# Performance work log

Hardware: AMD Instinct MI355X
Metric: run time of the kernel (lower is better)

## Reference

```python
import jax, jax.numpy as jnp
import numpy as np


def spmm(src, dst, w, x, n):
    # out[i] = sum_{e: dst[e]==i} w[e] * x[src[e]]  == th.spmm(adj, x) with adj COO (dst=row, src=col)
    return jax.ops.segment_sum(x[src] * w[:, None], dst, num_segments=n)


def gcn(x, ei, w, W1, b1, W2, b2):
    # GCN.forward: relu(gc1(x, adj)) -> dropout(eval: identity) -> gc2(x, adj)
    n = x.shape[0]
    src, dst = ei[1], ei[0]
    h = jax.nn.relu(spmm(src, dst, w, x @ W1, n) + b1)
    return spmm(src, dst, w, h @ W2, n) + b2


def setup_inputs() -> dict:
    key = jax.random.key(0)
    ks = jax.random.split(key, 24)
    Nd, Ns = 100000, 50000
    Fd, Fs, H1, H2 = 256, 256, 256, 128
    DEG = 32
    Ed, Es = Nd * DEG, Ns * DEG
    inp = {}
    inp['drug_sim_feat'] = jax.random.normal(ks[0], (Nd, Fd), jnp.float32)
    inp['drug_edge_index'] = jax.random.randint(ks[1], (2, Ed), 0, Nd, jnp.int32)
    inp['drug_edge_weight'] = jax.random.uniform(ks[2], (Ed,), jnp.float32) / DEG
    inp['drug_feat_edge_index'] = jax.random.randint(ks[3], (2, Ed), 0, Nd, jnp.int32)
    inp['drug_feat_edge_weight'] = jax.random.uniform(ks[4], (Ed,), jnp.float32) / DEG
    inp['disease_sim_feat'] = jax.random.normal(ks[5], (Ns, Fs), jnp.float32)
    inp['dis_edge_index'] = jax.random.randint(ks[6], (2, Es), 0, Ns, jnp.int32)
    inp['dis_edge_weight'] = jax.random.uniform(ks[7], (Es,), jnp.float32) / DEG
    inp['dis_feat_edge_index'] = jax.random.randint(ks[8], (2, Es), 0, Ns, jnp.int32)
    inp['dis_feat_edge_weight'] = jax.random.uniform(ks[9], (Es,), jnp.float32) / DEG
    # params: uniform(-stdv, stdv), stdv = 1/sqrt(out_features) as in reset_parameters
    def unif(k, shape, out_f):
        s = 1.0 / np.sqrt(out_f)
        return jax.random.uniform(k, shape, jnp.float32, -s, s)
    inp['W1d'] = unif(ks[10], (Fd, H1), H1); inp['b1d'] = unif(ks[11], (H1,), H1)
    inp['W2d'] = unif(ks[12], (H1, H2), H2); inp['b2d'] = unif(ks[13], (H2,), H2)
    inp['W1s'] = unif(ks[14], (Fs, H1), H1); inp['b1s'] = unif(ks[15], (H1,), H1)
    inp['W2s'] = unif(ks[16], (H1, H2), H2); inp['b2s'] = unif(ks[17], (H2,), H2)
    # fusion Linears (nhid2*2 -> nhid2); kaiming-ish uniform
    fs = 1.0 / np.sqrt(2 * H2)
    inp['Wfd'] = jax.random.uniform(ks[18], (2 * H2, H2), jnp.float32, -fs, fs)
    inp['bfd'] = jax.random.uniform(ks[19], (H2,), jnp.float32, -fs, fs)
    inp['Wfs'] = jax.random.uniform(ks[20], (2 * H2, H2), jnp.float32, -fs, fs)
    inp['bfs'] = jax.random.uniform(ks[21], (H2,), jnp.float32, -fs, fs)
    return inp


def reference(drug_sim_feat, drug_edge_index, drug_edge_weight,
              drug_feat_edge_index, drug_feat_edge_weight,
              disease_sim_feat, dis_edge_index, dis_edge_weight,
              dis_feat_edge_index, dis_feat_edge_weight,
              W1d, b1d, W2d, b2d, W1s, b1s, W2s, b2s,
              Wfd, bfd, Wfs, bfs):
    # dropout in eval mode (identity)
    emb1_sim = gcn(drug_sim_feat, drug_edge_index, drug_edge_weight, W1d, b1d, W2d, b2d)
    emb2_sim = gcn(disease_sim_feat, dis_edge_index, dis_edge_weight, W1s, b1s, W2s, b2s)
    emb1_feat = gcn(drug_sim_feat, drug_feat_edge_index, drug_feat_edge_weight, W1d, b1d, W2d, b2d)
    emb2_feat = gcn(disease_sim_feat, dis_feat_edge_index, dis_feat_edge_weight, W1s, b1s, W2s, b2s)
    emb1 = jax.nn.relu(jnp.concatenate([emb1_sim, emb1_feat], axis=1) @ Wfd + bfd)
    emb2 = jax.nn.relu(jnp.concatenate([emb2_sim, emb2_feat], axis=1) @ Wfs + bfs)
    return (emb1, emb2, emb1_sim, emb1_feat, emb2_sim, emb2_feat)
```

## Files before the change

### kernel.cpp

```cpp
#include <hip/hip_runtime.h>

typedef _Float16 f16;
typedef __attribute__((ext_vector_type(8))) _Float16 f16x8;
typedef __attribute__((ext_vector_type(4))) float f32x4;

__device__ inline ushort f2h_bits(float f) {
    f16 h = (f16)f;
    return __builtin_bit_cast(ushort, h);
}

struct T6 {
    const float* s[6];
    ushort* d[6];
    int N[6];
};

__global__ __launch_bounds__(256) void transpose6_k(T6 a) {
    __shared__ ushort tile[32][33];
    const int z = blockIdx.z;
    const int K = 256, N = a.N[z];
    int k0 = blockIdx.x * 32, n0 = blockIdx.y * 32;
    if (n0 >= N) return;
    const float* W = a.s[z];
    ushort* Wt = a.d[z];
    int tx = threadIdx.x & 31, ty = threadIdx.x >> 5;
    #pragma unroll
    for (int i = 0; i < 32; i += 8)
        tile[ty + i][tx] = f2h_bits(W[(size_t)(k0 + ty + i) * N + n0 + tx]);
    __syncthreads();
    #pragma unroll
    for (int i = 0; i < 32; i += 8)
        Wt[(size_t)(n0 + ty + i) * K + k0 + tx] = tile[tx][ty + i];
}

struct GraphDesc {
    const int* ei;
    const float* w;
    int E, n, NB, bstoff;
    int* row_ptr;
    int2* perm;
};
struct G4 { GraphDesc g[4]; };

__global__ __launch_bounds__(256) void hist_b(G4 a, int* __restrict__ bcounts) {
    const GraphDesc& G = a.g[blockIdx.y];
    const int e0 = blockIdx.x * 4096;
    if (e0 >= G.E) return;
    __shared__ int h[512];
    int t = threadIdx.x;
    h[t] = 0; h[t + 256] = 0;
    __syncthreads();
    #pragma unroll
    for (int k = 0; k < 16; ++k) {
        int i = e0 + t + k * 256;
        if (i < G.E) atomicAdd(&h[((uint)G.ei[i]) >> 8], 1);
    }
    __syncthreads();
    int* bc = bcounts + blockIdx.y * 512;
    for (int b = t; b < 512; b += 256)
        if (h[b]) atomicAdd(&bc[b], h[b]);
}

__global__ __launch_bounds__(256) void scan_b(G4 a, const int* __restrict__ bcounts,
                                              int* __restrict__ bbase, int* __restrict__ bcursor) {
    const int gidx = blockIdx.x;
    const GraphDesc& G = a.g[gidx];
    const int* bc = bcounts + gidx * 512;
    int* base = bbase + gidx * 513;
    int* cur  = bcursor + gidx * 512;
    int t = threadIdx.x, lane = t & 63, wave = t >> 6;
    int v0 = bc[2 * t], v1 = bc[2 * t + 1];
    int s = v0 + v1;
    int incl = s;
    for (int off = 1; off < 64; off <<= 1) {
        int u = __shfl_up(incl, off);
        if (lane >= off) incl += u;
    }
    __shared__ int wsum[4];
    if (lane == 63) wsum[wave] = incl;
    __syncthreads();
    int excl = incl - s;
    for (int wv = 0; wv < wave; ++wv) excl += wsum[wv];
    base[2 * t] = excl;      cur[2 * t] = excl;
    base[2 * t + 1] = excl + v0; cur[2 * t + 1] = excl + v0;
    if (t == 0) { base[512] = G.E; G.row_ptr[G.n] = G.E; }
}

__global__ __launch_bounds__(256) void scatter_b(G4 a, int* __restrict__ bcursor,
                                                 int2* __restrict__ bst) {
    const GraphDesc& G = a.g[blockIdx.y];
    const int e0 = blockIdx.x * 4096;
    if (e0 >= G.E) return;
    __shared__ int hist[512], excl[512], sbase[512], lcur[512];
    __shared__ int2 stage[4096];
    __shared__ ushort sbin[4096];
    const int t = threadIdx.x, lane = t & 63, wave = t >> 6;
    const int cnt = min(4096, G.E - e0);
    int* bcur = bcursor + blockIdx.y * 512;

    hist[t] = 0; hist[t + 256] = 0;
    __syncthreads();

    int   d[16], s[16];
    float wv[16];
    #pragma unroll
    for (int k = 0; k < 16; ++k) {
        int i = t + k * 256;
        if (i < cnt) {
            d[k]  = G.ei[e0 + i];
            s[k]  = G.ei[(size_t)G.E + e0 + i];
            wv[k] = G.w[e0 + i];
            atomicAdd(&hist[((uint)d[k]) >> 8], 1);
        }
    }
    __syncthreads();

    {
        int v0 = hist[2 * t], v1 = hist[2 * t + 1];
        int sum = v0 + v1;
        int incl = sum;
        for (int off = 1; off < 64; off <<= 1) {
            int u = __shfl_up(incl, off);
            if (lane >= off) incl += u;
        }
        __shared__ int wsum[4];
        if (lane == 63) wsum[wave] = incl;
        __syncthreads();
        int e = incl - sum;
        for (int wvv = 0; wvv < wave; ++wvv) e += wsum[wvv];
        excl[2 * t] = e; excl[2 * t + 1] = e + v0;
    }
    __syncthreads();

    for (int b = t; b < 512; b += 256) {
        int c = hist[b];
        sbase[b] = c ? atomicAdd(&bcur[b], c) : 0;
        lcur[b] = excl[b];
    }
    __syncthreads();

    #pragma unroll
    for (int k = 0; k < 16; ++k) {
        int i = t + k * 256;
        if (i < cnt) {
            int bin = ((uint)d[k]) >> 8;
            int pos = atomicAdd(&lcur[bin], 1);
            stage[pos] = make_int2((s[k] << 8) | (d[k] & 255), __float_as_int(wv[k]));
            sbin[pos] = (ushort)bin;
        }
    }
    __syncthreads();

    #pragma unroll
    for (int k = 0; k < 16; ++k) {
        int i = t + k * 256;
        if (i < cnt) {
            int2 r = stage[i];
            int bin = sbin[i];
            bst[(size_t)G.bstoff + sbase[bin] + i - excl[bin]] = r;
        }
    }
}

__global__ __launch_bounds__(256) void finalize_b(G4 a, const int* __restrict__ bbase,
                                                  const int2* __restrict__ bst) {
    const GraphDesc& G = a.g[blockIdx.y];
    const int b = blockIdx.x;
    if (b >= G.NB) return;
    __shared__ int hist[256], cur[256], wsum[4];
    const int t = threadIdx.x, lane = t & 63, wave = t >> 6;
    const int* base = bbase + blockIdx.y * 513;
    const int lo = base[b], hi = base[b + 1];
    const int2* bg = bst + G.bstoff;
    hist[t] = 0;
    __syncthreads();
    for (int i = lo + t; i < hi; i += 256)
        atomicAdd(&hist[bg[i].x & 255], 1);
    __syncthreads();
    int v = hist[t];
    int incl = v;
    for (int off = 1; off < 64; off <<= 1) {
        int u = __shfl_up(incl, off);
        if (lane >= off) incl += u;
    }
    if (lane == 63) wsum[wave] = incl;
    __syncthreads();
    int excl = incl - v;
    for (int wv = 0; wv < wave; ++wv) excl += wsum[wv];
    const int r0 = b << 8;
    const int nrows = min(256, G.n - r0);
    if (t < nrows) G.row_ptr[r0 + t] = lo + excl;
    cur[t] = lo + excl;
    __syncthreads();
    for (int i = lo + t; i < hi; i += 256) {
        int2 r = bg[i];
        int local = r.x & 255;
        int slot = atomicAdd(&cur[local], 1);
        G.perm[slot] = make_int2(r.x >> 8, r.y);
    }
}

template<int C, bool RELU, bool DUAL>
__global__ __launch_bounds__(256) void spmm_f16(
    const f16* __restrict__ x,
    const int2* __restrict__ perm,
    const int* __restrict__ row_ptr, const float* __restrict__ bias,
    ushort* __restrict__ out_h, float* __restrict__ out_f, int n)
{
    const int wave = threadIdx.x >> 6, lane = threadIdx.x & 63;
    const int row = blockIdx.x * 4 + wave;
    if (row >= n) return;
    const int F = 64 * C;
    const int e0 = row_ptr[row], e1 = row_ptr[row + 1];
    float acc[C] = {};
    const int laneoff = lane * C;

    for (int eb = e0; eb < e1; eb += 64) {
        int idx = eb + lane;
        int myS = 0; int myW = 0;
        if (idx < e1) { int2 rec = perm[idx]; myS = rec.x; myW = rec.y; }
        int m = min(64, e1 - eb);
        for (int j0 = 0; j0 < m; j0 += 8) {
            #pragma unroll
            for (int u = 0; u < 8; ++u) {
                int j = j0 + u;
                int   s = __builtin_amdgcn_readlane(myS, j);
                float w = __int_as_float(__builtin_amdgcn_readlane(myW, j));
                const f16* xr = x + (size_t)((uint)s * (uint)F) + laneoff;
                if (C == 4) {
                    union { uint2 u2; f16 h[4]; } cv;
                    cv.u2 = *reinterpret_cast<const uint2*>(xr);
                    acc[0] = fmaf((float)cv.h[0], w, acc[0]);
                    acc[1] = fmaf((float)cv.h[1], w, acc[1]);
                    acc[2] = fmaf((float)cv.h[2], w, acc[2]);
                    acc[3] = fmaf((float)cv.h[3], w, acc[3]);
                } else {
                    union { uint u1; f16 h[2]; } cv;
                    cv.u1 = *reinterpret_cast<const uint*>(xr);
                    acc[0] = fmaf((float)cv.h[0], w, acc[0]);
                    acc[1] = fmaf((float)cv.h[1], w, acc[1]);
                }
            }
        }
    }

    #pragma unroll
    for (int c = 0; c < C; ++c) {
        float v = acc[c] + bias[laneoff + c];
        acc[c] = RELU ? fmaxf(v, 0.f) : v;
    }
    size_t ob = (size_t)row * F + laneoff;
    if (DUAL) {
        if (C == 4) *reinterpret_cast<float4*>(out_f + ob) = make_float4(acc[0], acc[1], acc[2], acc[3]);
        else        *reinterpret_cast<float2*>(out_f + ob) = make_float2(acc[0], acc[1]);
    }
    if (C == 4) *reinterpret_cast<ushort4*>(out_h + ob) =
        make_ushort4(f2h_bits(acc[0]), f2h_bits(acc[1]), f2h_bits(acc[2]), f2h_bits(acc[3]));
    else        *reinterpret_cast<ushort2*>(out_h + ob) =
        make_ushort2(f2h_bits(acc[0]), f2h_bits(acc[1]));
}

template<bool CVTA, bool FUSE, bool RELU, bool BIAS, bool F32OUT>
__global__ __launch_bounds__(256) void gemm_mfma(
    const void* __restrict__ Av, const ushort* __restrict__ A2,
    const ushort* __restrict__ Bt, const float* __restrict__ bias,
    ushort* __restrict__ Ch, float* __restrict__ Cf,
    int M, int N, int K)
{
    __shared__ ushort Asb[128 * 32];
    __shared__ ushort Bsb[128 * 32];
    const int tid = threadIdx.x;
    const int lane = tid & 63, wave = tid >> 6;
    const int wr = wave >> 1, wc = wave & 1;
    const int bm = blockIdx.x * 128, bn = blockIdx.y * 128;

    f32x4 acc[4][4] = {};

    for (int k0 = 0; k0 < K; k0 += 32) {
        #pragma unroll
        for (int h = 0; h < 2; ++h) {
            int slot = tid + 256 * h;
            int r = slot >> 2, cb = slot & 3;
            int row = bm + r;
            uint4 v = make_uint4(0, 0, 0, 0);
            if (row < M) {
                int kk = k0 + cb * 8;
                if (CVTA) {
                    const float* Af = (const float*)Av;
                    float4 lo = *reinterpret_cast<const float4*>(Af + (size_t)row * K + kk);
                    float4 hi = *reinterpret_cast<const float4*>(Af + (size_t)row * K + kk + 4);
                    ushort h8[8] = { f2h_bits(lo.x), f2h_bits(lo.y), f2h_bits(lo.z), f2h_bits(lo.w),
                                     f2h_bits(hi.x), f2h_bits(hi.y), f2h_bits(hi.z), f2h_bits(hi.w) };
                    v = *reinterpret_cast<const uint4*>(h8);
                } else if (FUSE) {
                    const ushort* Ap = (kk < 128) ? (const ushort*)Av : A2;
                    v = *reinterpret_cast<const uint4*>(Ap + (size_t)row * 128 + (kk & 127));
                } else {
                    v = *reinterpret_cast<const uint4*>((const ushort*)Av + (size_t)row * K + kk);
                }
            }
            int scb = cb ^ ((r >> 1) & 3);
            *reinterpret_cast<uint4*>(&Asb[r * 32 + scb * 8]) = v;
        }
        #pragma unroll
        for (int h = 0; h < 2; ++h) {
            int slot = tid + 256 * h;
            int r = slot >> 2, cb = slot & 3;
            uint4 v = *reinterpret_cast<const uint4*>(Bt + (size_t)(bn + r) * K + k0 + cb * 8);
            int scb = cb ^ ((r >> 1) & 3);
            *reinterpret_cast<uint4*>(&Bsb[r * 32 + scb * 8]) = v;
        }
        __syncthreads();

        f16x8 fa[4], fb[4];
        #pragma unroll
        for (int i = 0; i < 4; ++i) {
            int r = wr * 64 + i * 16 + (lane & 15);
            int scb = (lane >> 4) ^ ((r >> 1) & 3);
            fa[i] = *reinterpret_cast<const f16x8*>(&Asb[r * 32 + scb * 8]);
        }
        #pragma unroll
        for (int j = 0; j < 4; ++j) {
            int r = wc * 64 + j * 16 + (lane & 15);
            int scb = (lane >> 4) ^ ((r >> 1) & 3);
            fb[j] = *reinterpret_cast<const f16x8*>(&Bsb[r * 32 + scb * 8]);
        }
        #pragma unroll
        for (int i = 0; i < 4; ++i)
            #pragma unroll
            for (int j = 0; j < 4; ++j)
                acc[i][j] = __builtin_amdgcn_mfma_f32_16x16x32_f16(fa[i], fb[j], acc[i][j], 0, 0, 0);
        __syncthreads();
    }

    #pragma unroll
    for (int i = 0; i < 4; ++i) {
        #pragma unroll
        for (int r4 = 0; r4 < 4; ++r4) {
            int row = bm + wr * 64 + i * 16 + (lane >> 4) * 4 + r4;
            if (row >= M) continue;
            #pragma unroll
            for (int j = 0; j < 4; ++j) {
                int col = bn + wc * 64 + j * 16 + (lane & 15);
                float v = acc[i][j][r4];
                if (BIAS) v += bias[col];
                if (RELU) v = fmaxf(v, 0.f);
                if (F32OUT) Cf[(size_t)row * N + col] = v;
                else        Ch[(size_t)row * N + col] = f2h_bits(v);
            }
        }
    }
}

extern "C" void kernel_launch(void* const* d_in, const int* in_sizes, int n_in,
                              void* d_out, int out_size, void* d_ws, size_t ws_size,
                              hipStream_t stream) {
    const float* Xd       = (const float*)d_in[0];
    const int*   eid_sim  = (const int*)  d_in[1];
    const float* wd_sim   = (const float*)d_in[2];
    const int*   eid_feat = (const int*)  d_in[3];
    const float* wd_feat  = (const float*)d_in[4];
    const float* Xs       = (const float*)d_in[5];
    const int*   eis_sim  = (const int*)  d_in[6];
    const float* ws_sim   = (const float*)d_in[7];
    const int*   eis_feat = (const int*)  d_in[8];
    const float* ws_feat  = (const float*)d_in[9];
    const float* W1d = (const float*)d_in[10]; const float* b1d = (const float*)d_in[11];
    const float* W2d = (const float*)d_in[12]; const float* b2d = (const float*)d_in[13];
    const float* W1s = (const float*)d_in[14]; const float* b1s = (const float*)d_in[15];
    const float* W2s = (const float*)d_in[16]; const float* b2s = (const float*)d_in[17];
    const float* Wfd = (const float*)d_in[18]; const float* bfd = (const float*)d_in[19];
    const float* Wfs = (const float*)d_in[20]; const float* bfs = (const float*)d_in[21];

    const int Fd = 256, H1 = 256, H2 = 128;
    const int Nd = in_sizes[0] / Fd;
    const int Ns = in_sizes[5] / Fd;
    const int Ed = in_sizes[2];
    const int Es = in_sizes[7];

    float* out    = (float*)d_out;
    float* o_emb1 = out;
    float* o_emb2 = o_emb1 + (size_t)Nd * H2;
    float* o_e1s  = o_emb2 + (size_t)Ns * H2;
    float* o_e1f  = o_e1s  + (size_t)Nd * H2;
    float* o_e2s  = o_e1f  + (size_t)Nd * H2;
    float* o_e2f  = o_e2s  + (size_t)Ns * H2;

    char* p = (char*)d_ws;
    auto alloc = [&](size_t bytes) { char* q = p; p += (bytes + 255) & ~(size_t)255; return q; };
    ushort* xw1   = (ushort*)alloc((size_t)Nd * 256 * 2);
    ushort* hbuf  = (ushort*)alloc((size_t)Nd * 256 * 2);
    ushort* tbuf  = (ushort*)alloc((size_t)Nd * 128 * 2);
    ushort* es_h  = (ushort*)alloc((size_t)Nd * 128 * 2);
    ushort* ef_h  = (ushort*)alloc((size_t)Nd * 128 * 2);
    ushort* W1dt  = (ushort*)alloc(256 * 256 * 2);
    ushort* W2dt  = (ushort*)alloc(256 * 128 * 2);
    ushort* Wfdt  = (ushort*)alloc(256 * 128 * 2);
    ushort* W1st  = (ushort*)alloc(256 * 256 * 2);
    ushort* W2st  = (ushort*)alloc(256 * 128 * 2);
    ushort* Wfst  = (ushort*)alloc(256 * 128 * 2);
    int2*   perm0 = (int2*)alloc((size_t)Ed * 8);
    int2*   perm1 = (int2*)alloc((size_t)Ed * 8);
    int2*   perm2 = (int2*)alloc((size_t)Es * 8);
    int2*   perm3 = (int2*)alloc((size_t)Es * 8);
    int*    rp0   = (int*) alloc((size_t)(Nd + 1) * 4);
    int*    rp1   = (int*) alloc((size_t)(Nd + 1) * 4);
    int*    rp2   = (int*) alloc((size_t)(Ns + 1) * 4);
    int*    rp3   = (int*) alloc((size_t)(Ns + 1) * 4);
    int*    bcounts = (int*)alloc(4 * 512 * 4);
    int*    bbase   = (int*)alloc(4 * 513 * 4);
    int*    bcursor = (int*)alloc(4 * 512 * 4);
    int2*   bst     = (int2*)xw1;

    {
        T6 a;
        a.s[0] = W1d; a.s[1] = W2d; a.s[2] = Wfd; a.s[3] = W1s; a.s[4] = W2s; a.s[5] = Wfs;
        a.d[0] = W1dt; a.d[1] = W2dt; a.d[2] = Wfdt; a.d[3] = W1st; a.d[4] = W2st; a.d[5] = Wfst;
        a.N[0] = 256; a.N[1] = 128; a.N[2] = 128; a.N[3] = 256; a.N[4] = 128; a.N[5] = 128;
        transpose6_k<<<dim3(8, 8, 6), 256, 0, stream>>>(a);
    }

    G4 a;
    a.g[0] = { eid_sim,  wd_sim,  Ed, Nd, (Nd + 255) >> 8, 0,           rp0, perm0 };
    a.g[1] = { eid_feat, wd_feat, Ed, Nd, (Nd + 255) >> 8, Ed,          rp1, perm1 };
    a.g[2] = { eis_sim,  ws_sim,  Es, Ns, (Ns + 255) >> 8, 2 * Ed,      rp2, perm2 };
    a.g[3] = { eis_feat, ws_feat, Es, Ns, (Ns + 255) >> 8, 2 * Ed + Es, rp3, perm3 };
    {
        const int maxEB = (Ed + 4095) / 4096;
        const int maxNB = (Nd + 255) >> 8;
        hipMemsetAsync(bcounts, 0, 4 * 512 * 4, stream);
        hist_b<<<dim3(maxEB, 4), 256, 0, stream>>>(a, bcounts);
        scan_b<<<4, 256, 0, stream>>>(a, bcounts, bbase, bcursor);
        scatter_b<<<dim3(maxEB, 4), 256, 0, stream>>>(a, bcursor, bst);
        finalize_b<<<dim3(maxNB, 4), 256, 0, stream>>>(a, bbase, bst);
    }

    auto branch = [&](const float* X, int n,
                      const int2* pA, const int* rpA,
                      const int2* pB, const int* rpB,
                      const ushort* W1t, const float* b1,
                      const ushort* W2t, const float* b2,
                      const ushort* Wft, const float* bfu,
                      float* o_sim, float* o_feat, float* o_emb) {
        gemm_mfma<true, false, false, false, false><<<dim3((n + 127) / 128, 2), 256, 0, stream>>>(
            X, nullptr, W1t, nullptr, xw1, nullptr, n, 256, 256);
        const int2* pm[2] = {pA, pB};
        const int*  rp[2] = {rpA, rpB};
        float*      of[2] = {o_sim, o_feat};
        ushort*     oh[2] = {es_h, ef_h};
        for (int g = 0; g < 2; ++g) {
            spmm_f16<4, true, false><<<(n + 3) / 4, 256, 0, stream>>>(
                (const f16*)xw1, pm[g], rp[g], b1, hbuf, nullptr, n);
            gemm_mfma<false, false, false, false, false><<<dim3((n + 127) / 128, 1), 256, 0, stream>>>(
                hbuf, nullptr, W2t, nullptr, tbuf, nullptr, n, 128, 256);
            spmm_f16<2, false, true><<<(n + 3) / 4, 256, 0, stream>>>(
                (const f16*)tbuf, pm[g], rp[g], b2, oh[g], of[g], n);
        }
        gemm_mfma<false, true, true, true, true><<<dim3((n + 127) / 128, 1), 256, 0, stream>>>(
            es_h, ef_h, Wft, bfu, nullptr, o_emb, n, 128, 256);
    };

    branch(Xd, Nd, perm0, rp0, perm1, rp1,
           W1dt, b1d, W2dt, b2d, Wfdt, bfd, o_e1s, o_e1f, o_emb1);
    branch(Xs, Ns, perm2, rp2, perm3, rp3,
           W1st, b1s, W2st, b2s, Wfst, bfs, o_e2s, o_e2f, o_emb2);
}
```

Measured before the change: 1.384 ms.

## Batch both graphs' layer-1 SpMM into one launch and swap GEMM grid order

The two layer-1 SpMMs, which share the same XW1 input, now run as a single launch with blockIdx.y selecting the graph, writing into separate h buffers so both graphs gather from XW1 in the same window. The first GEMM's grid is swapped so the two N-tiles of one M block run adjacently and can share the A rows. The SpMM kernel is split into specialised layer-1 and layer-2 versions. Workspace is reshuffled to make room for the second h/t buffers, which adds memory footprint and aliases es_h/ef_h onto xw1.

```diff
diff --git a/kernel.cpp b/kernel.cpp
--- a/kernel.cpp
+++ b/kernel.cpp
@@ -200,18 +200,24 @@
     }
 }
 
-template<int C, bool RELU, bool DUAL>
-__global__ __launch_bounds__(256) void spmm_f16(
-    const f16* __restrict__ x,
-    const int2* __restrict__ perm,
-    const int* __restrict__ row_ptr, const float* __restrict__ bias,
-    ushort* __restrict__ out_h, float* __restrict__ out_f, int n)
+struct PairDesc {
+    const int2* perm[2];
+    const int*  rp[2];
+    ushort*     outh[2];
+};
+
+template<int C>
+__global__ __launch_bounds__(256) void spmm_pair_f16(
+    const f16* __restrict__ x, PairDesc a, const float* __restrict__ bias, int n)
 {
+    const int g = blockIdx.y;
     const int wave = threadIdx.x >> 6, lane = threadIdx.x & 63;
     const int row = blockIdx.x * 4 + wave;
     if (row >= n) return;
+    const int2* __restrict__ perm = a.perm[g];
+    const int*  __restrict__ rp   = a.rp[g];
     const int F = 64 * C;
-    const int e0 = row_ptr[row], e1 = row_ptr[row + 1];
+    const int e0 = rp[row], e1 = rp[row + 1];
     float acc[C] = {};
     const int laneoff = lane * C;
 
@@ -227,19 +233,12 @@
                 int   s = __builtin_amdgcn_readlane(myS, j);
                 float w = __int_as_float(__builtin_amdgcn_readlane(myW, j));
                 const f16* xr = x + (size_t)((uint)s * (uint)F) + laneoff;
-                if (C == 4) {
-                    union { uint2 u2; f16 h[4]; } cv;
-                    cv.u2 = *reinterpret_cast<const uint2*>(xr);
-                    acc[0] = fmaf((float)cv.h[0], w, acc[0]);
-                    acc[1] = fmaf((float)cv.h[1], w, acc[1]);
-                    acc[2] = fmaf((float)cv.h[2], w, acc[2]);
-                    acc[3] = fmaf((float)cv.h[3], w, acc[3]);
-                } else {
-                    union { uint u1; f16 h[2]; } cv;
-                    cv.u1 = *reinterpret_cast<const uint*>(xr);
-                    acc[0] = fmaf((float)cv.h[0], w, acc[0]);
-                    acc[1] = fmaf((float)cv.h[1], w, acc[1]);
-                }
+                union { uint2 u2; f16 h[4]; } cv;
+                cv.u2 = *reinterpret_cast<const uint2*>(xr);
+                acc[0] = fmaf((float)cv.h[0], w, acc[0]);
+                acc[1] = fmaf((float)cv.h[1], w, acc[1]);
+                acc[2] = fmaf((float)cv.h[2], w, acc[2]);
+                acc[3] = fmaf((float)cv.h[3], w, acc[3]);
             }
         }
     }
@@ -247,20 +246,53 @@
     #pragma unroll
     for (int c = 0; c < C; ++c) {
         float v = acc[c] + bias[laneoff + c];
-        acc[c] = RELU ? fmaxf(v, 0.f) : v;
-    }
+        acc[c] = fmaxf(v, 0.f);
+    }
+    *reinterpret_cast<ushort4*>(a.outh[g] + (size_t)row * F + laneoff) =
+        make_ushort4(f2h_bits(acc[0]), f2h_bits(acc[1]), f2h_bits(acc[2]), f2h_bits(acc[3]));
+}
+
+__global__ __launch_bounds__(256) void spmm_l2_f16(
+    const f16* __restrict__ x,
+    const int2* __restrict__ perm,
+    const int* __restrict__ row_ptr, const float* __restrict__ bias,
+    ushort* __restrict__ out_h, float* __restrict__ out_f, int n)
+{
+    const int wave = threadIdx.x >> 6, lane = threadIdx.x & 63;
+    const int row = blockIdx.x * 4 + wave;
+    if (row >= n) return;
+    const int F = 128;
+    const int e0 = row_ptr[row], e1 = row_ptr[row + 1];
+    float acc[2] = {};
+    const int laneoff = lane * 2;
+
+    for (int eb = e0; eb < e1; eb += 64) {
+        int idx = eb + lane;
+        int myS = 0; int myW = 0;
+        if (idx < e1) { int2 rec = perm[idx]; myS = rec.x; myW = rec.y; }
+        int m = min(64, e1 - eb);
+        for (int j0 = 0; j0 < m; j0 += 8) {
+            #pragma unroll
+            for (int u = 0; u < 8; ++u) {
+                int j = j0 + u;
+                int   s = __builtin_amdgcn_readlane(myS, j);
+                float w = __int_as_float(__builtin_amdgcn_readlane(myW, j));
+                union { uint u1; f16 h[2]; } cv;
+                cv.u1 = *reinterpret_cast<const uint*>(x + (size_t)((uint)s * (uint)F) + laneoff);
+                acc[0] = fmaf((float)cv.h[0], w, acc[0]);
+                acc[1] = fmaf((float)cv.h[1], w, acc[1]);
+            }
+        }
+    }
+
+    acc[0] += bias[laneoff];
+    acc[1] += bias[laneoff + 1];
     size_t ob = (size_t)row * F + laneoff;
-    if (DUAL) {
-        if (C == 4) *reinterpret_cast<float4*>(out_f + ob) = make_float4(acc[0], acc[1], acc[2], acc[3]);
-        else        *reinterpret_cast<float2*>(out_f + ob) = make_float2(acc[0], acc[1]);
-    }
-    if (C == 4) *reinterpret_cast<ushort4*>(out_h + ob) =
-        make_ushort4(f2h_bits(acc[0]), f2h_bits(acc[1]), f2h_bits(acc[2]), f2h_bits(acc[3]));
-    else        *reinterpret_cast<ushort2*>(out_h + ob) =
-        make_ushort2(f2h_bits(acc[0]), f2h_bits(acc[1]));
-}
-
-template<bool CVTA, bool FUSE, bool RELU, bool BIAS, bool F32OUT>
+    *reinterpret_cast<float2*>(out_f + ob) = make_float2(acc[0], acc[1]);
+    *reinterpret_cast<ushort2*>(out_h + ob) = make_ushort2(f2h_bits(acc[0]), f2h_bits(acc[1]));
+}
+
+template<bool SWAP, bool CVTA, bool FUSE, bool RELU, bool BIAS, bool F32OUT>
 __global__ __launch_bounds__(256) void gemm_mfma(
     const void* __restrict__ Av, const ushort* __restrict__ A2,
     const ushort* __restrict__ Bt, const float* __restrict__ bias,
@@ -272,7 +304,8 @@
     const int tid = threadIdx.x;
     const int lane = tid & 63, wave = tid >> 6;
     const int wr = wave >> 1, wc = wave & 1;
-    const int bm = blockIdx.x * 128, bn = blockIdx.y * 128;
+    const int bm = (SWAP ? blockIdx.y : blockIdx.x) * 128;
+    const int bn = (SWAP ? blockIdx.x : blockIdx.y) * 128;
 
     f32x4 acc[4][4] = {};
 
@@ -389,10 +422,10 @@
     char* p = (char*)d_ws;
     auto alloc = [&](size_t bytes) { char* q = p; p += (bytes + 255) & ~(size_t)255; return q; };
     ushort* xw1   = (ushort*)alloc((size_t)Nd * 256 * 2);
-    ushort* hbuf  = (ushort*)alloc((size_t)Nd * 256 * 2);
-    ushort* tbuf  = (ushort*)alloc((size_t)Nd * 128 * 2);
-    ushort* es_h  = (ushort*)alloc((size_t)Nd * 128 * 2);
-    ushort* ef_h  = (ushort*)alloc((size_t)Nd * 128 * 2);
+    ushort* hbuf0 = (ushort*)alloc((size_t)Nd * 256 * 2);
+    ushort* hbuf1 = (ushort*)alloc((size_t)Nd * 256 * 2);
+    ushort* tbuf0 = (ushort*)alloc((size_t)Nd * 128 * 2);
+    ushort* tbuf1 = (ushort*)alloc((size_t)Nd * 128 * 2);
     ushort* W1dt  = (ushort*)alloc(256 * 256 * 2);
     ushort* W2dt  = (ushort*)alloc(256 * 128 * 2);
     ushort* Wfdt  = (ushort*)alloc(256 * 128 * 2);
@@ -410,7 +443,9 @@
     int*    bcounts = (int*)alloc(4 * 512 * 4);
     int*    bbase   = (int*)alloc(4 * 513 * 4);
     int*    bcursor = (int*)alloc(4 * 512 * 4);
-    int2*   bst     = (int2*)xw1;
+    int2*   bst  = (int2*)hbuf0;
+    ushort* es_h = xw1;
+    ushort* ef_h = xw1 + (size_t)Nd * 128;
 
     {
         T6 a;
@@ -442,21 +477,24 @@
                       const ushort* W2t, const float* b2,
                       const ushort* Wft, const float* bfu,
                       float* o_sim, float* o_feat, float* o_emb) {
-        gemm_mfma<true, false, false, false, false><<<dim3((n + 127) / 128, 2), 256, 0, stream>>>(
+        const int Mb = (n + 127) / 128;
+        gemm_mfma<true, true, false, false, false, false><<<dim3(2, Mb), 256, 0, stream>>>(
             X, nullptr, W1t, nullptr, xw1, nullptr, n, 256, 256);
-        const int2* pm[2] = {pA, pB};
-        const int*  rp[2] = {rpA, rpB};
-        float*      of[2] = {o_sim, o_feat};
-        ushort*     oh[2] = {es_h, ef_h};
-        for (int g = 0; g < 2; ++g) {
-            spmm_f16<4, true, false><<<(n + 3) / 4, 256, 0, stream>>>(
-                (const f16*)xw1, pm[g], rp[g], b1, hbuf, nullptr, n);
-            gemm_mfma<false, false, false, false, false><<<dim3((n + 127) / 128, 1), 256, 0, stream>>>(
-                hbuf, nullptr, W2t, nullptr, tbuf, nullptr, n, 128, 256);
-            spmm_f16<2, false, true><<<(n + 3) / 4, 256, 0, stream>>>(
-                (const f16*)tbuf, pm[g], rp[g], b2, oh[g], of[g], n);
-        }
-        gemm_mfma<false, true, true, true, true><<<dim3((n + 127) / 128, 1), 256, 0, stream>>>(
+        PairDesc pd;
+        pd.perm[0] = pA; pd.perm[1] = pB;
+        pd.rp[0] = rpA;  pd.rp[1] = rpB;
+        pd.outh[0] = hbuf0; pd.outh[1] = hbuf1;
+        spmm_pair_f16<4><<<dim3((n + 3) / 4, 2), 256, 0, stream>>>(
+            (const f16*)xw1, pd, b1, n);
+        gemm_mfma<false, false, false, false, false, false><<<dim3(Mb, 1), 256, 0, stream>>>(
+            hbuf0, nullptr, W2t, nullptr, tbuf0, nullptr, n, 128, 256);
+        gemm_mfma<false, false, false, false, false, false><<<dim3(Mb, 1), 256, 0, stream>>>(
+            hbuf1, nullptr, W2t, nullptr, tbuf1, nullptr, n, 128, 256);
+        spmm_l2_f16<<<(n + 3) / 4, 256, 0, stream>>>(
+            (const f16*)tbuf0, pA, rpA, b2, es_h, o_sim, n);
+        spmm_l2_f16<<<(n + 3) / 4, 256, 0, stream>>>(
+            (const f16*)tbuf1, pB, rpB, b2, ef_h, o_feat, n);
+        gemm_mfma<false, false, true, true, true, true><<<dim3(Mb, 1), 256, 0, stream>>>(
             es_h, ef_h, Wft, bfu, nullptr, o_emb, n, 128, 256);
     };
 
```

Measured after the change: 1.379 ms (median of 2 runs). About the same (-0.4%).
